# Kernel tuning notes

Measured on AMD Instinct MI355X. Metric: run time of the kernel, lower is better.

## Reference

```python
import jax, jax.numpy as jnp
import numpy as np

B, S, E = 2, 1024, 768
H, D = 12, 64          # num_heads, head_dim
M = 768                # mlp_hidden_size
Q = 4                  # q_stride
EPS = 1e-5


def _layernorm(x, w, b):
    mu = x.mean(-1, keepdims=True)
    var = ((x - mu) ** 2).mean(-1, keepdims=True)
    return (x - mu) * jax.lax.rsqrt(var + EPS) * w + b


def setup_inputs() -> dict:
    key = jax.random.key(0)
    ks = jax.random.split(key, 16)
    s = 0.02
    d = {
        'x': jax.random.normal(ks[0], (B, S, E), jnp.float32),
        'ln1_w': jnp.ones((E,), jnp.float32), 'ln1_b': jnp.zeros((E,), jnp.float32),
        'Wq': jax.random.normal(ks[1], (E, E), jnp.float32) * s, 'bq': jnp.zeros((E,), jnp.float32),
        'Wk': jax.random.normal(ks[2], (E, E), jnp.float32) * s, 'bk': jnp.zeros((E,), jnp.float32),
        'Wv': jax.random.normal(ks[3], (E, E), jnp.float32) * s, 'bv': jnp.zeros((E,), jnp.float32),
        'Wo': jax.random.normal(ks[4], (E, E), jnp.float32) * s, 'bo': jnp.zeros((E,), jnp.float32),
        'pond': jnp.zeros((), jnp.float32),  # ponderation_param
        'ln2_w': jnp.ones((E,), jnp.float32), 'ln2_b': jnp.zeros((E,), jnp.float32),
        'fc1_W': jax.random.normal(ks[5], (Q * M, E), jnp.float32) * s, 'fc1_b': jnp.zeros((Q * M,), jnp.float32),
        'vqc_W': jax.random.normal(ks[6], (M, M), jnp.float32) * s, 'vqc_b': jnp.zeros((M,), jnp.float32),
        'fc2_W': jax.random.normal(ks[7], (E, Q * M), jnp.float32) * s, 'fc2_b': jnp.zeros((E,), jnp.float32),
    }
    return d


def reference(x, ln1_w, ln1_b, Wq, bq, Wk, bk, Wv, bv, Wo, bo, pond,
              ln2_w, ln2_b, fc1_W, fc1_b, vqc_W, vqc_b, fc2_W, fc2_b):
    # --- attention sublayer ---
    h = _layernorm(x, ln1_w, ln1_b)
    def heads(W, b):
        return (h @ W.T + b).reshape(B, S, H, D).transpose(0, 2, 1, 3)  # [B,H,S,D]
    q, k, v = heads(Wq, bq), heads(Wk, bk), heads(Wv, bv)

    # N=2: einsum with identity A reduces to q k^T
    logits = jnp.einsum('bhid,bhjd->bhij', q, k) / jnp.sqrt(jnp.float32(D))
    attn = jax.nn.softmax(logits, axis=-1)  # dropout is identity at inference

    # RBF similarity blending ('linear' ponderation)
    q_norm = (q ** 2).sum(-1, keepdims=True)                  # [B,H,S,1]
    k_norm = (k ** 2).sum(-1, keepdims=True).swapaxes(-2, -1)  # [B,H,1,S]
    d2 = jnp.maximum(q_norm + k_norm - 2.0 * jnp.einsum('bhid,bhjd->bhij', q, k), 0.0)
    sigma2 = jnp.clip(q_norm, 1e-8, 1e4)
    rbf = jnp.exp(-d2 / sigma2)
    rbf = rbf / jnp.maximum(rbf.sum(-1, keepdims=True), 1e-8)
    rbf = jnp.nan_to_num(rbf, nan=0.0, posinf=0.0, neginf=0.0)
    s_val = jax.nn.sigmoid(pond)
    p0, p1 = 1.0 - s_val, s_val
    attn = (p0 * attn + p1 * rbf) / (p0 + p1 + 1e-7)

    vals = jnp.einsum('bhij,bhjd->bhid', attn, v)
    vals = vals.transpose(0, 2, 1, 3).reshape(B, S, E)
    x = x + (vals @ Wo.T + bo)

    # --- sliced MLP sublayer (q_stride=4, overlapping offset-1 slices) ---
    y = _layernorm(x, ln2_w, ln2_b)
    h1 = y @ fc1_W.T + fc1_b                                  # [B,S,Q*M]
    slices = jnp.stack([h1[:, :, i:i + M] for i in range(Q)], axis=2)  # [B,S,Q,M]
    z = slices @ vqc_W.T + vqc_b                              # vqc (linear fallback)
    z = z.transpose(0, 1, 3, 2).reshape(B, S, Q * M)          # permute(0,1,3,2).view
    z = jax.nn.gelu(z, approximate=False)
    out = z @ fc2_W.T + fc2_b
    return x + out
```

## Files before the change

kernel.cpp:

```cpp
#include <hip/hip_runtime.h>
#include <math.h>

#define E_DIM 768
#define S_LEN 1024
#define B_SZ 2
#define H_CNT 12
#define D_HEAD 64
#define M_DIM 768
#define Q_STRIDE 4
#define N_FC1 771

typedef __attribute__((ext_vector_type(8))) short bf16x8;
typedef __attribute__((ext_vector_type(4))) float f32x4;

#define AS1 __attribute__((address_space(1)))
#define AS3 __attribute__((address_space(3)))

__device__ __forceinline__ void gld_lds16(void* lds, const void* g) {
    __builtin_amdgcn_global_load_lds((const AS1 void*)g, (AS3 void*)lds, 16, 0, 0);
}

__device__ __forceinline__ short f2bf(float f) {
    unsigned u = __float_as_uint(f);
    unsigned r = (u + 0x7fffu + ((u >> 16) & 1u)) >> 16;
    return (short)r;
}

__device__ __forceinline__ float bf2f(short s) {
    return __uint_as_float(((unsigned)(unsigned short)s) << 16);
}


__device__ __forceinline__ float block_reduce_sum(float v, volatile float* red) {
#pragma unroll
    for (int off = 32; off > 0; off >>= 1) v += __shfl_xor(v, off);
    __syncthreads();
    if ((threadIdx.x & 63) == 0) red[threadIdx.x >> 6] = v;
    __syncthreads();
    return red[0] + red[1] + red[2] + red[3];
}


__global__ __launch_bounds__(256) void preamble(
        const float* __restrict__ Wq, const float* __restrict__ Wk,
        const float* __restrict__ Wv, const float* __restrict__ Wo,
        const float* __restrict__ fc1W, const float* __restrict__ vqcW,
        const float* __restrict__ fc2W, short* __restrict__ dst,
        const float* __restrict__ bq, const float* __restrict__ bk,
        const float* __restrict__ bv, float* __restrict__ bqkv,
        const float* __restrict__ x, const float* __restrict__ ln1_w,
        const float* __restrict__ ln1_b, short* __restrict__ actb) {
    __shared__ float red[4];
    int tid = threadIdx.x;
    if (blockIdx.x < 2048) {
        int row = blockIdx.x;
        const float* xr = x + (size_t)row * E_DIM;
        float v0 = xr[tid], v1 = xr[tid + 256], v2 = xr[tid + 512];
        float s = block_reduce_sum(v0 + v1 + v2, red);
        float mu = s * (1.0f / E_DIM);
        float d0 = v0 - mu, d1 = v1 - mu, d2 = v2 - mu;
        float var = block_reduce_sum(d0 * d0 + d1 * d1 + d2 * d2, red) * (1.0f / E_DIM);
        float rs = rsqrtf(var + 1e-5f);
        short* orow = actb + (size_t)row * E_DIM;
        orow[tid]       = f2bf(d0 * rs * ln1_w[tid]       + ln1_b[tid]);
        orow[tid + 256] = f2bf(d1 * rs * ln1_w[tid + 256] + ln1_b[tid + 256]);
        orow[tid + 512] = f2bf(d2 * rs * ln1_w[tid + 512] + ln1_b[tid + 512]);
        return;
    }
    if (blockIdx.x == 2048) {
#pragma unroll
        for (int u = 0; u < 9; u++) {
            int i = tid + u * 256;
            float v = (i < 768) ? bq[i] : (i < 1536) ? bk[i - 768] : bv[i - 1536];
            bqkv[i] = v;
        }
        return;
    }
    int t = (blockIdx.x - 2049) * 256 + tid;
    if (t >= 1475136) return;
    int e = t * 4;
    const float* src; int off;
    if      (e < 589824)  { src = Wq;   off = e; }
    else if (e < 1179648) { src = Wk;   off = e - 589824; }
    else if (e < 1769472) { src = Wv;   off = e - 1179648; }
    else if (e < 2359296) { src = Wo;   off = e - 1769472; }
    else if (e < 2951424) { src = fc1W; off = e - 2359296; }
    else if (e < 3541248) { src = vqcW; off = e - 2951424; }
    else                  { src = fc2W; off = e - 3541248; }
    float4 v = *(const float4*)(src + off);
    short4 o = make_short4(f2bf(v.x), f2bf(v.y), f2bf(v.z), f2bf(v.w));
    *(short4*)(dst + e) = o;
}


template <int OUTMODE, int MR>
__global__ __launch_bounds__(256, 2) void gemm_bf16(
        const short* __restrict__ A, int lda,
        const short* __restrict__ W, int ldw,
        const float* __restrict__ bias,
        void* __restrict__ outp, int ldo, size_t spitch,
        short* __restrict__ Kfp, short* __restrict__ Vfp,
        int N, int klen, int dogelu) {
    constexpr int MI = MR / 32;
    constexpr int AH = MR * 32;
    constexpr int NA = MR / 64;
    constexpr int ASL = 2 * AH;
    __shared__ short At[2 * ASL];
    __shared__ short Bt[2 * 8192];
    const int tid = threadIdx.x;
    const int lane = tid & 63;
    const int wave = tid >> 6;
    const int wr = (wave >> 1) * (MI * 16);
    const int wc = (wave & 1) * 64;
    const int ml = lane & 15;
    const int kq = lane >> 4;
    const int row0 = blockIdx.y * MR;
    const int col0 = blockIdx.x * 128;
    const int kbase = blockIdx.z * klen;

    const short* Ag[NA]; int aoff[NA];
#pragma unroll
    for (int u = 0; u < NA; u++) {
        int c = tid + u * 256;
        int am = c >> 2, ak = ((c & 3) ^ ((am >> 1) & 3)) * 8;
        Ag[u] = A + (size_t)(row0 + am) * lda + ak + kbase;
        aoff[u] = c * 8;
    }
    const int c0 = tid, c1 = tid + 256;
    const int bm0 = c0 >> 2, bk0 = (((c0 & 3) ^ ((bm0 >> 1) & 3))) * 8;
    const int bm1 = c1 >> 2, bk1 = (((c1 & 3) ^ ((bm1 >> 1) & 3))) * 8;
    int wrow0 = col0 + bm0; if (wrow0 > N - 1) wrow0 = N - 1;
    int wrow1 = col0 + bm1; if (wrow1 > N - 1) wrow1 = N - 1;
    const short* Wg0 = W + (size_t)wrow0 * ldw + bk0 + kbase;
    const short* Wg1 = W + (size_t)wrow1 * ldw + bk1 + kbase;

    const int kxor = (kq ^ ((ml >> 1) & 3)) * 8;

    f32x4 acc[MI][4];
#pragma unroll
    for (int i = 0; i < MI; i++)
#pragma unroll
        for (int j = 0; j < 4; j++) acc[i][j] = {0.f, 0.f, 0.f, 0.f};

    auto stage = [&](int buf, int k0) {
        short* Ab = At + buf * ASL;
        short* Bb = Bt + buf * 8192;
#pragma unroll
        for (int u = 0; u < NA; u++) {
            gld_lds16(Ab + aoff[u], Ag[u] + k0);
            gld_lds16(Ab + AH + aoff[u], Ag[u] + k0 + 32);
        }
        gld_lds16(Bb + c0 * 8, Wg0 + k0);
        gld_lds16(Bb + c1 * 8, Wg1 + k0);
        gld_lds16(Bb + 4096 + c0 * 8, Wg0 + k0 + 32);
        gld_lds16(Bb + 4096 + c1 * 8, Wg1 + k0 + 32);
    };

    stage(0, 0);
    int cur = 0;
    for (int k0 = 0; k0 < klen; k0 += 64) {
        __syncthreads();
        if (k0 + 64 < klen) stage(cur ^ 1, k0 + 64);
        const short* Ac = At + cur * ASL;
        const short* Bc = Bt + cur * 8192;
#pragma unroll
        for (int half = 0; half < 2; half++) {
            const short* Ah = Ac + half * AH;
            const short* Bh = Bc + half * 4096;
            bf16x8 af[MI], bfr[4];
#pragma unroll
            for (int i = 0; i < MI; i++)
                af[i] = *(const bf16x8*)&Ah[(wr + i * 16 + ml) * 32 + kxor];
#pragma unroll
            for (int j = 0; j < 4; j++)
                bfr[j] = *(const bf16x8*)&Bh[(wc + j * 16 + ml) * 32 + kxor];
#pragma unroll
            for (int i = 0; i < MI; i++)
#pragma unroll
                for (int j = 0; j < 4; j++)
                    acc[i][j] = __builtin_amdgcn_mfma_f32_16x16x32_bf16(af[i], bfr[j], acc[i][j], 0, 0, 0);
        }
        cur ^= 1;
    }

#pragma unroll
    for (int i = 0; i < MI; i++) {
#pragma unroll
        for (int j = 0; j < 4; j++) {
#pragma unroll
            for (int rr = 0; rr < 4; rr++) {
                int r = row0 + wr + i * 16 + kq * 4 + rr;
                int c = col0 + wc + j * 16 + ml;
                if (c < N) {
                    float v = acc[i][j][rr];
                    if (OUTMODE < 4) v += bias[c];
                    if (OUTMODE == 2 && dogelu)
                        v = 0.5f * v * (1.0f + erff(v * 0.70710678118654752f));
                    if (OUTMODE == 2) {
                        ((short*)outp)[(size_t)(r >> 2) * ldo + c * 4 + (r & 3)] = f2bf(v);
                    } else if (OUTMODE == 5) {
                        ((short*)outp)[blockIdx.z * spitch + (size_t)r * ldo + c] = f2bf(v);
                    } else if (OUTMODE == 3) {
                        int s = r & 1023, bb = r >> 10;
                        if (c < 768) {
                            ((short*)outp)[(size_t)r * 768 + c] = f2bf(v);
                        } else if (c < 1536) {
                            int df = c - 768; int hh = df >> 6, d = df & 63;
                            int bh2 = bb * 12 + hh;
                            size_t idx = ((size_t)(bh2 * 64 + (s >> 4)) * 2 + (d >> 5)) * 512
                                       + (size_t)((d >> 3) & 3) * 128 + (size_t)(s & 15) * 8 + (d & 7);
                            Kfp[idx] = f2bf(v);
                        } else {
                            int df = c - 1536; int hh = df >> 6, d = df & 63;
                            int bh2 = bb * 12 + hh;
                            size_t idx = ((size_t)(bh2 * 32 + (s >> 5))) * 2048
                                       + (size_t)(d >> 4) * 512 + (size_t)((s >> 3) & 3) * 128
                                       + (size_t)(d & 15) * 8 + (s & 7);
                            Vfp[idx] = f2bf(v);
                        }
                    }
                }
            }
        }
    }
}


__global__ __launch_bounds__(256) void reduce_wo_ln(
        const short* __restrict__ part, const float* __restrict__ bo,
        const float* __restrict__ x, const float* __restrict__ w,
        const float* __restrict__ bvec, float* __restrict__ x2,
        short* __restrict__ y) {
    __shared__ float red[4];
    int row = blockIdx.x, tid = threadIdx.x;
    const size_t SP = (size_t)2048 * 768;
    const short* pr = part + (size_t)row * 768;
    const float* xr = x + (size_t)row * 768;
    float* x2r = x2 + (size_t)row * 768;
    float v[3];
#pragma unroll
    for (int u = 0; u < 3; u++) {
        int c = tid + u * 256;
        float s = bo[c] + xr[c];
#pragma unroll
        for (int z = 0; z < 4; z++) s += bf2f(pr[z * SP + c]);
        v[u] = s; x2r[c] = s;
    }
    float s = block_reduce_sum(v[0] + v[1] + v[2], red);
    float mu = s * (1.0f / 768.f);
    float d0 = v[0] - mu, d1 = v[1] - mu, d2 = v[2] - mu;
    float var = block_reduce_sum(d0 * d0 + d1 * d1 + d2 * d2, red) * (1.0f / 768.f);
    float rs = rsqrtf(var + 1e-5f);
    short* orow = y + (size_t)row * 768;
    orow[tid]       = f2bf(d0 * rs * w[tid]       + bvec[tid]);
    orow[tid + 256] = f2bf(d1 * rs * w[tid + 256] + bvec[tid + 256]);
    orow[tid + 512] = f2bf(d2 * rs * w[tid + 512] + bvec[tid + 512]);
}

__global__ __launch_bounds__(256) void reduce_fc1_expand(
        const short* __restrict__ part, const float* __restrict__ b,
        const short* __restrict__ y, const short* __restrict__ w768,
        short* __restrict__ Avqc) {
    __shared__ float row[772];
    __shared__ float red[4];
    int r = blockIdx.x, tid = threadIdx.x;
    const size_t SP = (size_t)2048 * 768;
    const short* pr = part + (size_t)r * 768;
#pragma unroll
    for (int u = 0; u < 3; u++) {
        int c = tid + u * 256;
        float s = b[c];
#pragma unroll
        for (int z = 0; z < 4; z++) s += bf2f(pr[z * SP + c]);
        row[c] = s;
    }
    const short* yr = y + (size_t)r * 768;
    float y0 = bf2f(yr[tid]), y1 = bf2f(yr[tid + 256]), y2 = bf2f(yr[tid + 512]);
#pragma unroll
    for (int k = 0; k < 3; k++) {
        const short* wk = w768 + k * 768;
        float s = y0 * bf2f(wk[tid]) + y1 * bf2f(wk[tid + 256]) + y2 * bf2f(wk[tid + 512]);
        s = block_reduce_sum(s, red);
        if (tid == 0) row[768 + k] = s + b[768 + k];
    }
    __syncthreads();
#pragma unroll
    for (int q = 0; q < 4; q++) {
        short* orow = Avqc + (size_t)(r * 4 + q) * 768;
#pragma unroll
        for (int u = 0; u < 3; u++) {
            int m = tid + u * 256;
            orow[m] = f2bf(row[m + q]);
        }
    }
}

__global__ __launch_bounds__(256) void reduce_fc2(
        const short* __restrict__ part, const float* __restrict__ b,
        const float* __restrict__ x2, float* __restrict__ out) {
    int t = blockIdx.x * 256 + threadIdx.x;
    int row = t / 192;
    int c = (t - row * 192) * 4;
    size_t off = (size_t)row * 768 + c;
    const size_t SP = (size_t)2048 * 768;
    float4 bb = *(const float4*)(b + c);
    float4 xx = *(const float4*)(x2 + off);
    float o0 = bb.x + xx.x, o1 = bb.y + xx.y, o2 = bb.z + xx.z, o3 = bb.w + xx.w;
#pragma unroll
    for (int z = 0; z < 4; z++) {
        short4 v = *(const short4*)(part + z * SP + off);
        o0 += bf2f(v.x); o1 += bf2f(v.y); o2 += bf2f(v.z); o3 += bf2f(v.w);
    }
    float4 o = make_float4(o0, o1, o2, o3);
    *(float4*)(out + off) = o;
}


__global__ __launch_bounds__(256, 4) void attn_mfma(
        const short* __restrict__ Qb,
        const short* __restrict__ Kf,
        const short* __restrict__ Vf,
        const float* __restrict__ pond,
        short* __restrict__ vals) {
    __shared__ __align__(16) short Pbuf[2 * 4 * 16 * 72];
    __shared__ float qn_l[4][16];
    __shared__ float is_l[4][16];
    __shared__ float esx[2][16], rsx[2][16];

    const int tid = threadIdx.x;
    const int lane = tid & 63;
    const int wave = tid >> 6;
    const int wq = wave & 1;
    const int wp = wave >> 1;
    const int ml = lane & 15;
    const int kq = lane >> 4;

    const int fid = blockIdx.x;
    const int w = (fid & 7) * 96 + (fid >> 3);
    const int qt2 = w & 31;
    const int bh = w >> 5;
    const int b = (bh >= 12) ? 1 : 0;
    const int h = bh - b * 12;

    const int qrow = b * S_LEN + qt2 * 32 + wq * 16 + ml;
    const short* qp = Qb + (size_t)qrow * 768 + h * 64 + kq * 8;
    bf16x8 aq0 = *(const bf16x8*)qp;
    bf16x8 aq1 = *(const bf16x8*)(qp + 32);

    float qn_part = 0.f;
#pragma unroll
    for (int e = 0; e < 8; e++) {
        float v0 = bf2f(aq0[e]), v1 = bf2f(aq1[e]);
        qn_part += v0 * v0 + v1 * v1;
    }
    qn_part += __shfl_xor(qn_part, 16);
    qn_part += __shfl_xor(qn_part, 32);
    if (kq == 0) {
        qn_l[wave][ml] = qn_part;
        float sig = fminf(fmaxf(qn_part, 1e-8f), 1e4f);
        is_l[wave][ml] = 1.0f / sig;
    }
    __syncthreads();

    float qn_r[4], is_r[4];
#pragma unroll
    for (int r = 0; r < 4; r++) {
        qn_r[r] = qn_l[wave][kq * 4 + r];
        is_r[r] = is_l[wave][kq * 4 + r];
    }

    f32x4 Oe[4], Or[4];
#pragma unroll
    for (int dt = 0; dt < 4; dt++) { Oe[dt] = {0.f,0.f,0.f,0.f}; Or[dt] = {0.f,0.f,0.f,0.f}; }
    float es_p[4] = {0.f,0.f,0.f,0.f}, rs_p[4] = {0.f,0.f,0.f,0.f};

    const short* KfB = Kf + (size_t)bh * 65536;
    const short* VfB = Vf + (size_t)bh * 65536;
    short* PeW = Pbuf + wave * 1152;
    short* PrW = Pbuf + 4608 + wave * 1152;

    for (int it = 0; it < 8; it++) {
        const short* Kit = KfB + (size_t)(it + 8 * wp) * 4096;
        const short* Vit = VfB + (size_t)(it + 8 * wp) * 4096;

#pragma unroll
        for (int jtl = 0; jtl < 4; jtl++) {
            bf16x8 bk0 = *(const bf16x8*)&Kit[(jtl * 2 + 0) * 512 + lane * 8];
            bf16x8 bk1 = *(const bf16x8*)&Kit[(jtl * 2 + 1) * 512 + lane * 8];
            float knp = 0.f;
#pragma unroll
            for (int e = 0; e < 8; e++) {
                float k0v = bf2f(bk0[e]), k1v = bf2f(bk1[e]);
                knp += k0v * k0v + k1v * k1v;
            }
            knp += __shfl_xor(knp, 16);
            knp += __shfl_xor(knp, 32);
            f32x4 c = {0.f,0.f,0.f,0.f};
            c = __builtin_amdgcn_mfma_f32_16x16x32_bf16(aq0, bk0, c, 0, 0, 0);
            c = __builtin_amdgcn_mfma_f32_16x16x32_bf16(aq1, bk1, c, 0, 0, 0);
#pragma unroll
            for (int r = 0; r < 4; r++) {
                float qk = c[r];
                float e = __expf(qk * 0.125f);
                float tt = (2.f * qk - qn_r[r] - knp) * is_r[r];
                float rb = fminf(__expf(tt), 1.0f);
                es_p[r] += e; rs_p[r] += rb;
                PeW[(kq * 4 + r) * 72 + jtl * 16 + ml] = f2bf(e);
                PrW[(kq * 4 + r) * 72 + jtl * 16 + ml] = f2bf(rb);
            }
        }

#pragma unroll
        for (int jcl = 0; jcl < 2; jcl++) {
            bf16x8 pa_e = *(const bf16x8*)&PeW[ml * 72 + jcl * 32 + kq * 8];
            bf16x8 pa_r = *(const bf16x8*)&PrW[ml * 72 + jcl * 32 + kq * 8];
#pragma unroll
            for (int dt = 0; dt < 4; dt++) {
                bf16x8 bv = *(const bf16x8*)&Vit[(jcl * 4 + dt) * 512 + lane * 8];
                Oe[dt] = __builtin_amdgcn_mfma_f32_16x16x32_bf16(pa_e, bv, Oe[dt], 0, 0, 0);
                Or[dt] = __builtin_amdgcn_mfma_f32_16x16x32_bf16(pa_r, bv, Or[dt], 0, 0, 0);
            }
        }
    }

#pragma unroll
    for (int off = 1; off <= 8; off <<= 1) {
#pragma unroll
        for (int r = 0; r < 4; r++) {
            es_p[r] += __shfl_xor(es_p[r], off);
            rs_p[r] += __shfl_xor(rs_p[r], off);
        }
    }

    __syncthreads();
    float* cb = (float*)Pbuf;
    if (wp == 1) {
        float* cl = cb + (size_t)(wq * 64 + lane) * 32;
#pragma unroll
        for (int dt = 0; dt < 4; dt++)
#pragma unroll
            for (int r = 0; r < 4; r++) {
                cl[dt * 4 + r] = Oe[dt][r];
                cl[16 + dt * 4 + r] = Or[dt][r];
            }
        if (ml == 0) {
#pragma unroll
            for (int r = 0; r < 4; r++) {
                esx[wq][kq * 4 + r] = es_p[r];
                rsx[wq][kq * 4 + r] = rs_p[r];
            }
        }
    }
    __syncthreads();
    if (wp == 0) {
        float p = pond[0];
        float sv = 1.0f / (1.0f + __expf(-p));
        float p0 = 1.0f - sv, p1 = sv;
        float blendinv = 1.0f / (p0 + p1 + 1e-7f);
        const float* cl = cb + (size_t)(wq * 64 + lane) * 32;
        float we[4], wr[4];
#pragma unroll
        for (int r = 0; r < 4; r++) {
            float es = es_p[r] + esx[wq][kq * 4 + r];
            float rs = rs_p[r] + rsx[wq][kq * 4 + r];
            we[r] = p0 * blendinv / es;
            wr[r] = p1 * blendinv / fmaxf(rs, 1e-8f);
        }
#pragma unroll
        for (int dt = 0; dt < 4; dt++) {
#pragma unroll
            for (int r = 0; r < 4; r++) {
                float oe = Oe[dt][r] + cl[dt * 4 + r];
                float orr = Or[dt][r] + cl[16 + dt * 4 + r];
                float v = oe * we[r] + orr * wr[r];
                int token = b * S_LEN + qt2 * 32 + wq * 16 + kq * 4 + r;
                vals[(size_t)token * 768 + h * 64 + dt * 16 + ml] = f2bf(v);
            }
        }
    }
}


extern "C" void kernel_launch(void* const* d_in, const int* in_sizes, int n_in,
                              void* d_out, int out_size, void* d_ws, size_t ws_size,
                              hipStream_t stream) {
    const float* x     = (const float*)d_in[0];
    const float* ln1_w = (const float*)d_in[1];
    const float* ln1_b = (const float*)d_in[2];
    const float* Wq    = (const float*)d_in[3];
    const float* bq    = (const float*)d_in[4];
    const float* Wk    = (const float*)d_in[5];
    const float* bk    = (const float*)d_in[6];
    const float* Wv    = (const float*)d_in[7];
    const float* bv    = (const float*)d_in[8];
    const float* Wo    = (const float*)d_in[9];
    const float* bo    = (const float*)d_in[10];
    const float* pond  = (const float*)d_in[11];
    const float* ln2_w = (const float*)d_in[12];
    const float* ln2_b = (const float*)d_in[13];
    const float* fc1_W = (const float*)d_in[14];
    const float* fc1_b = (const float*)d_in[15];
    const float* vqc_W = (const float*)d_in[16];
    const float* vqc_b = (const float*)d_in[17];
    const float* fc2_W = (const float*)d_in[18];
    const float* fc2_b = (const float*)d_in[19];
    float* out = (float*)d_out;

    char* p = (char*)d_ws;
    short* Qb   = (short*)p;  p += (size_t)2048 * 768 * 2;
    short* Kfb  = (short*)p;  p += (size_t)2048 * 768 * 2;
    short* Vfb  = (short*)p;  p += (size_t)2048 * 768 * 2;
    float* x2   = (float*)p;  p += (size_t)2048 * 768 * 4;
    float* bqkv = (float*)p;  p += 2304 * 4;
    short* actb = (short*)p;  p += (size_t)2048 * 768 * 2;
    short* g    = (short*)p;  p += (size_t)2048 * 3072 * 2;
    short* Avqc = (short*)p;  p += (size_t)8192 * 768 * 2;
    short* partb = (short*)p; p += (size_t)4 * 2048 * 768 * 2;
    short* wreg = (short*)p;  p += (size_t)5900544 * 2;
    short* Wqkvb = wreg;
    short* Wob   = wreg + 1769472;
    short* fc1b  = wreg + 2359296;
    short* vqcb  = wreg + 2951424;
    short* fc2b  = wreg + 3541248;

    dim3 blk(256);
    const size_t SP = (size_t)2048 * 768;

    preamble<<<7812, blk, 0, stream>>>(Wq, Wk, Wv, Wo, fc1_W, vqc_W, fc2_W, wreg,
                                       bq, bk, bv, bqkv, x, ln1_w, ln1_b, actb);
    gemm_bf16<3, 64><<<dim3(18, 32, 1), blk, 0, stream>>>(actb, 768, Wqkvb, 768, bqkv,
                                                          Qb, 768, 0, Kfb, Vfb, 2304, 768, 0);
    attn_mfma<<<768, blk, 0, stream>>>(Qb, Kfb, Vfb, pond, actb);
    gemm_bf16<5, 64><<<dim3(6, 32, 4), blk, 0, stream>>>(actb, 768, Wob, 768, nullptr,
                                                         partb, 768, SP,
                                                         nullptr, nullptr, 768, 192, 0);
    reduce_wo_ln<<<2048, blk, 0, stream>>>(partb, bo, x, ln2_w, ln2_b, x2, actb);
    gemm_bf16<5, 64><<<dim3(6, 32, 4), blk, 0, stream>>>(actb, 768, fc1b, 768, nullptr,
                                                         partb, 768, SP,
                                                         nullptr, nullptr, 768, 192, 0);
    reduce_fc1_expand<<<2048, blk, 0, stream>>>(partb, fc1_b, actb, fc1b + 768 * 768, Avqc);
    gemm_bf16<2, 64><<<dim3(6, 128, 1), blk, 0, stream>>>(Avqc, 768, vqcb, 768, vqc_b,
                                                          g, 3072, 0, nullptr, nullptr, 768, 768, 1);
    gemm_bf16<5, 64><<<dim3(6, 32, 4), blk, 0, stream>>>(g, 3072, fc2b, 3072, nullptr,
                                                         partb, 768, SP,
                                                         nullptr, nullptr, 768, 768, 0);
    reduce_fc2<<<1536, blk, 0, stream>>>(partb, fc2_b, x2, out);
}
```

Before: 159.6 us.

## Split attention KV across four waves per 16-query tile, doubling grid

Each attention block now handles one 16-row query tile, and its four waves each process a quarter of the key/value sequence. Before, a block handled 32 query rows with the KV range split in two. Partial outputs and row sums from waves 1-3 are reduced through LDS into wave 0. The grid doubles to 1536 blocks and launch bounds rise to 6 blocks per CU, aiming for more parallelism and latency hiding on the attention stage. The LDS q-norm exchange and its barrier are replaced by wave shuffles. In exchange, K/V tiles are loaded once per 16 query rows instead of once per 32, and the cross-wave reduction grows.

```diff
diff --git a/kernel.cpp b/kernel.cpp
--- a/kernel.cpp
+++ b/kernel.cpp
@@ -316,33 +316,30 @@
 }
 
 
-__global__ __launch_bounds__(256, 4) void attn_mfma(
+__global__ __launch_bounds__(256, 6) void attn_mfma(
         const short* __restrict__ Qb,
         const short* __restrict__ Kf,
         const short* __restrict__ Vf,
         const float* __restrict__ pond,
         short* __restrict__ vals) {
-    __shared__ __align__(16) short Pbuf[2 * 4 * 16 * 72];
-    __shared__ float qn_l[4][16];
-    __shared__ float is_l[4][16];
-    __shared__ float esx[2][16], rsx[2][16];
+    __shared__ __align__(16) short Pbuf[12288];
+    __shared__ float esx[3][16], rsx[3][16];
 
     const int tid = threadIdx.x;
     const int lane = tid & 63;
     const int wave = tid >> 6;
-    const int wq = wave & 1;
-    const int wp = wave >> 1;
+    const int wp = wave;
     const int ml = lane & 15;
     const int kq = lane >> 4;
 
     const int fid = blockIdx.x;
-    const int w = (fid & 7) * 96 + (fid >> 3);
-    const int qt2 = w & 31;
-    const int bh = w >> 5;
+    const int w = (fid & 7) * 192 + (fid >> 3);
+    const int qt = w & 63;
+    const int bh = w >> 6;
     const int b = (bh >= 12) ? 1 : 0;
     const int h = bh - b * 12;
 
-    const int qrow = b * S_LEN + qt2 * 32 + wq * 16 + ml;
+    const int qrow = b * S_LEN + qt * 16 + ml;
     const short* qp = Qb + (size_t)qrow * 768 + h * 64 + kq * 8;
     bf16x8 aq0 = *(const bf16x8*)qp;
     bf16x8 aq1 = *(const bf16x8*)(qp + 32);
@@ -355,18 +352,11 @@
     }
     qn_part += __shfl_xor(qn_part, 16);
     qn_part += __shfl_xor(qn_part, 32);
-    if (kq == 0) {
-        qn_l[wave][ml] = qn_part;
-        float sig = fminf(fmaxf(qn_part, 1e-8f), 1e4f);
-        is_l[wave][ml] = 1.0f / sig;
-    }
-    __syncthreads();
-
     float qn_r[4], is_r[4];
 #pragma unroll
     for (int r = 0; r < 4; r++) {
-        qn_r[r] = qn_l[wave][kq * 4 + r];
-        is_r[r] = is_l[wave][kq * 4 + r];
+        qn_r[r] = __shfl(qn_part, kq * 4 + r);
+        is_r[r] = 1.0f / fminf(fmaxf(qn_r[r], 1e-8f), 1e4f);
     }
 
     f32x4 Oe[4], Or[4];
@@ -379,9 +369,9 @@
     short* PeW = Pbuf + wave * 1152;
     short* PrW = Pbuf + 4608 + wave * 1152;
 
-    for (int it = 0; it < 8; it++) {
-        const short* Kit = KfB + (size_t)(it + 8 * wp) * 4096;
-        const short* Vit = VfB + (size_t)(it + 8 * wp) * 4096;
+    for (int it = 0; it < 4; it++) {
+        const short* Kit = KfB + (size_t)(wp * 4 + it) * 4096;
+        const short* Vit = VfB + (size_t)(wp * 4 + it) * 4096;
 
 #pragma unroll
         for (int jtl = 0; jtl < 4; jtl++) {
@@ -434,20 +424,20 @@
 
     __syncthreads();
     float* cb = (float*)Pbuf;
-    if (wp == 1) {
-        float* cl = cb + (size_t)(wq * 64 + lane) * 32;
+    if (wp) {
+        float* cl = cb + (wp - 1) * 64 + lane;
 #pragma unroll
         for (int dt = 0; dt < 4; dt++)
 #pragma unroll
             for (int r = 0; r < 4; r++) {
-                cl[dt * 4 + r] = Oe[dt][r];
-                cl[16 + dt * 4 + r] = Or[dt][r];
+                cl[(dt * 4 + r) * 192] = Oe[dt][r];
+                cl[(16 + dt * 4 + r) * 192] = Or[dt][r];
             }
         if (ml == 0) {
 #pragma unroll
             for (int r = 0; r < 4; r++) {
-                esx[wq][kq * 4 + r] = es_p[r];
-                rsx[wq][kq * 4 + r] = rs_p[r];
+                esx[wp - 1][kq * 4 + r] = es_p[r];
+                rsx[wp - 1][kq * 4 + r] = rs_p[r];
             }
         }
     }
@@ -457,12 +447,11 @@
         float sv = 1.0f / (1.0f + __expf(-p));
         float p0 = 1.0f - sv, p1 = sv;
         float blendinv = 1.0f / (p0 + p1 + 1e-7f);
-        const float* cl = cb + (size_t)(wq * 64 + lane) * 32;
         float we[4], wr[4];
 #pragma unroll
         for (int r = 0; r < 4; r++) {
-            float es = es_p[r] + esx[wq][kq * 4 + r];
-            float rs = rs_p[r] + rsx[wq][kq * 4 + r];
+            float es = es_p[r] + esx[0][kq * 4 + r] + esx[1][kq * 4 + r] + esx[2][kq * 4 + r];
+            float rs = rs_p[r] + rsx[0][kq * 4 + r] + rsx[1][kq * 4 + r] + rsx[2][kq * 4 + r];
             we[r] = p0 * blendinv / es;
             wr[r] = p1 * blendinv / fmaxf(rs, 1e-8f);
         }
@@ -470,10 +459,13 @@
         for (int dt = 0; dt < 4; dt++) {
 #pragma unroll
             for (int r = 0; r < 4; r++) {
-                float oe = Oe[dt][r] + cl[dt * 4 + r];
-                float orr = Or[dt][r] + cl[16 + dt * 4 + r];
+                int e0 = dt * 4 + r;
+                float oe = Oe[dt][r] + cb[e0 * 192 + lane] + cb[e0 * 192 + 64 + lane]
+                         + cb[e0 * 192 + 128 + lane];
+                float orr = Or[dt][r] + cb[(16 + e0) * 192 + lane] + cb[(16 + e0) * 192 + 64 + lane]
+                          + cb[(16 + e0) * 192 + 128 + lane];
                 float v = oe * we[r] + orr * wr[r];
-                int token = b * S_LEN + qt2 * 32 + wq * 16 + kq * 4 + r;
+                int token = b * S_LEN + qt * 16 + kq * 4 + r;
                 vals[(size_t)token * 768 + h * 64 + dt * 16 + ml] = f2bf(v);
             }
         }
@@ -530,7 +522,7 @@
                                        bq, bk, bv, bqkv, x, ln1_w, ln1_b, actb);
     gemm_bf16<3, 64><<<dim3(18, 32, 1), blk, 0, stream>>>(actb, 768, Wqkvb, 768, bqkv,
                                                           Qb, 768, 0, Kfb, Vfb, 2304, 768, 0);
-    attn_mfma<<<768, blk, 0, stream>>>(Qb, Kfb, Vfb, pond, actb);
+    attn_mfma<<<1536, blk, 0, stream>>>(Qb, Kfb, Vfb, pond, actb);
     gemm_bf16<5, 64><<<dim3(6, 32, 4), blk, 0, stream>>>(actb, 768, Wob, 768, nullptr,
                                                          partb, 768, SP,
                                                          nullptr, nullptr, 768, 192, 0);
```

Result: slower. 179.7 us (+12.6%).
